# Performance work log

Hardware: AMD Instinct MI355X
Metric: run time of the kernel (lower is better)

The kernel has to match this reference:

```python
import jax, jax.numpy as jnp
import numpy as np

G, S, F, H, C, L = 32, 2048, 128, 128, 40, 3
N = G * S           # 65536 nodes
E = N * 16          # 1048576 edges


def setup_inputs() -> dict:
    key = jax.random.key(0)
    ks = jax.random.split(key, 10)
    x = jax.random.normal(ks[0], (N, F), dtype=jnp.float32)
    edge_index = jax.random.randint(ks[1], (2, E), 0, N, dtype=jnp.int64)
    E_meta = jax.random.normal(ks[2], (G, H), dtype=jnp.float32)
    ptr = (jnp.arange(G + 1, dtype=jnp.int64) * S)  # uniform partitions
    # learned params (xavier-ish scaling)
    w0 = jax.random.normal(ks[3], (F, 1), dtype=jnp.float32) * (2.0 / (F + 1)) ** 0.5
    b0 = jax.random.normal(ks[4], (F, H), dtype=jnp.float32) * (2.0 / (F + H)) ** 0.5
    conv_w = jax.random.normal(ks[5], (L, H, H), dtype=jnp.float32) * (1.0 / H) ** 0.5
    conv_b = jnp.zeros((L, H), dtype=jnp.float32)
    lt1_w = jax.random.normal(ks[6], (C, H), dtype=jnp.float32) * (1.0 / H) ** 0.5
    lt1_b = jnp.zeros((C,), dtype=jnp.float32)
    return {"x": x, "edge_index": edge_index, "E_meta": E_meta, "ptr": ptr,
            "w0": w0, "b0": b0, "conv_w": conv_w, "conv_b": conv_b,
            "lt1_w": lt1_w, "lt1_b": lt1_b}


def _gcn_conv(h, src, dst, deg_inv_sqrt, W, b):
    # GCNConv (PyG defaults): h' = D^-1/2 (A+I) D^-1/2 (h W) + b
    hw = h @ W                                          # [N,H]
    norm = deg_inv_sqrt[src] * deg_inv_sqrt[dst]        # [E+N]
    msg = hw[src] * norm[:, None]                       # gather + scale
    return jax.ops.segment_sum(msg, dst, num_segments=h.shape[0]) + b


def reference(x, edge_index, E_meta, ptr, w0, b0, conv_w, conv_b, lt1_w, lt1_b):
    n_nodes = x.shape[0]
    g = E_meta.shape[0]
    s = n_nodes // g  # uniform ptr (ptr[i] = i*s) by construction
    # per-partition dynamic weight: relu(w0 @ emb^T + b0) -> [G,F,H]
    Wdyn = jax.nn.relu(w0[None, :, :] * E_meta[:, None, :] + b0[None, :, :])
    # segment matmul x[ptr[i]:ptr[i+1]] @ Wdyn[i], concatenated -> [N,H]
    h = jnp.einsum('gsf,gfh->gsh', x.reshape(g, s, -1), Wdyn).reshape(n_nodes, -1)
    # add self loops once; symmetric normalization on target degree
    loop = jnp.arange(n_nodes, dtype=edge_index.dtype)
    src = jnp.concatenate([edge_index[0], loop])
    dst = jnp.concatenate([edge_index[1], loop])
    deg = jax.ops.segment_sum(jnp.ones_like(dst, dtype=h.dtype), dst,
                              num_segments=n_nodes)
    deg_inv_sqrt = jnp.where(deg > 0, jax.lax.rsqrt(deg), 0.0)
    for l in range(conv_w.shape[0]):
        h = jax.nn.relu(_gcn_conv(h, src, dst, deg_inv_sqrt, conv_w[l], conv_b[l]))
        # F.dropout with training=False is identity (eval mode)
    logits = h @ lt1_w.T + lt1_b
    return jax.nn.log_softmax(logits, axis=1)
```

## Files before the change

kernel.cpp:

```cpp
#include <hip/hip_runtime.h>

#define NNODES 65536
#define NEDGES 1048576
#define HDIM 128
#define NCLS 40
#define BCAP 6144

#define FP8_SCALE 32.0f
#define FP8_INV   0.03125f

typedef unsigned int uint;
typedef __attribute__((ext_vector_type(8))) short bf16x8;
typedef __attribute__((ext_vector_type(4))) float f32x4;
typedef __attribute__((ext_vector_type(2))) float f32x2;

__device__ __forceinline__ float bf_lo(uint v) {
    return __builtin_bit_cast(float, v << 16);
}
__device__ __forceinline__ float bf_hi(uint v) {
    return __builtin_bit_cast(float, v & 0xffff0000u);
}
__device__ __forceinline__ uint pack_bf16x2(float a, float b) {
    uint ua = __builtin_bit_cast(uint, a);
    uint ub = __builtin_bit_cast(uint, b);
    ua += 0x7fff + ((ua >> 16) & 1);
    ub += 0x7fff + ((ub >> 16) & 1);
    return (ua >> 16) | (ub & 0xffff0000u);
}
__device__ __forceinline__ float tobf(float v) {
    uint u = __builtin_bit_cast(uint, v);
    u += 0x7fff + ((u >> 16) & 1);
    return __builtin_bit_cast(float, u & 0xffff0000u);
}

__device__ __forceinline__ f32x2 fp8_pair(uint u) {
    return __builtin_amdgcn_cvt_pk_f32_fp8((int)u, false);
}

__global__ __launch_bounds__(256) void convT_kernel(
    const float* __restrict__ cw, uint* __restrict__ WT, int* __restrict__ gcursor,
    const float* __restrict__ ltw, uint* __restrict__ WcT8)
{
    int t = threadIdx.x;
    if (blockIdx.x == 0) gcursor[t] = 0;
    int idx = blockIdx.x * 256 + t;
    if (idx < 24576) {
        int ip = idx & 63;
        int o = (idx >> 6) & 127;
        int l = idx >> 13;
        int i0 = ip * 2;
        float v0 = cw[l * 16384 + i0 * 128 + o];
        float v1 = cw[l * 16384 + (i0 + 1) * 128 + o];
        WT[idx] = pack_bf16x2(v0, v1);
    } else {
        int idx2 = idx - 24576;
        int part = (idx2 >= 3072) ? 1 : 0;
        int r = idx2 - part * 3072;
        int o = r >> 6;
        int ip = r & 63;
        float v0 = 0.f, v1 = 0.f;
        if (o < NCLS) {
            float w0v = ltw[o * 128 + ip * 2];
            float w1v = ltw[o * 128 + ip * 2 + 1];
            float h0 = tobf(w0v), h1 = tobf(w1v);
            if (part == 0) { v0 = h0; v1 = h1; }
            else { v0 = w0v - h0; v1 = w1v - h1; }
        }
        WcT8[idx2] = pack_bf16x2(v0, v1);
    }
}

__global__ __launch_bounds__(256) void bucket_scatter(
    const int* __restrict__ src, const int* __restrict__ dst,
    int* __restrict__ gcursor, uint* __restrict__ binned)
{
    __shared__ int lcnt[256];
    __shared__ int lbase[256];
    int t = threadIdx.x;
    int base = blockIdx.x * 4096;
    lcnt[t] = 0;
    __syncthreads();
    uint e[16];
#pragma unroll
    for (int k = 0; k < 16; k++) {
        int i = base + k * 256 + t;
        uint s = (uint)src[i];
        uint d = (uint)dst[i];
        e[k] = (d << 16) | s;
        atomicAdd(&lcnt[d >> 8], 1);
    }
    __syncthreads();
    lbase[t] = t * BCAP + atomicAdd(&gcursor[t], lcnt[t]);
    lcnt[t] = 0;
    __syncthreads();
#pragma unroll
    for (int k = 0; k < 16; k++) {
        int b = e[k] >> 24;
        int r = atomicAdd(&lcnt[b], 1);
        binned[lbase[b] + r] = e[k];
    }
}

__global__ __launch_bounds__(256) void prep_kernel(
    const uint* __restrict__ binned, const int* __restrict__ gcursor,
    int* __restrict__ row_beg, int* __restrict__ row_end4,
    float* __restrict__ dis, int* __restrict__ csr,
    const float* __restrict__ w0, const float* __restrict__ em,
    const float* __restrict__ b0, const uint* __restrict__ convwT0,
    uint* __restrict__ WT)
{
    __shared__ int cnt[256];
    __shared__ int tmp[256];
    __shared__ int fb[256];
    const int t = threadIdx.x;

    if (blockIdx.x < 256) {
        int b = blockIdx.x;
        int e0 = b * BCAP, e1 = e0 + gcursor[b];
        cnt[t] = 0;
        __syncthreads();
        for (int i = e0 + t; i < e1; i += 256)
            atomicAdd(&cnt[(binned[i] >> 16) & 255], 1);
        __syncthreads();
        int v = cnt[t];
        int size4 = (v + 3) & ~3;
        tmp[t] = size4;
        __syncthreads();
        for (int off = 1; off < 256; off <<= 1) {
            int u = (t >= off) ? tmp[t - off] : 0;
            __syncthreads();
            tmp[t] += u;
            __syncthreads();
        }
        fb[t] = tmp[t] - size4;
        int node = (b << 8) + t;
        int beg = e0 + fb[t];
        row_beg[node] = beg;
        row_end4[node] = beg + size4;
        dis[node] = rsqrtf((float)(v + 1));
        for (int p = v; p < size4; p++) csr[beg + p] = NNODES;
        cnt[t] = 0;
        __syncthreads();
        for (int i = e0 + t; i < e1; i += 256) {
            uint e = binned[i];
            int d = (e >> 16) & 255;
            int r = atomicAdd(&cnt[d], 1);
            csr[e0 + fb[d] + r] = (int)(e & 0xffffu);
        }
    } else {
        int bb = blockIdx.x - 256;
        const int g = bb >> 3;
        const int c = bb & 7;
        const int wave = t >> 6;
        const int lane = t & 63;
        const int q = lane >> 4;
        const int l16 = lane & 15;
        const float* emg = em + g * 128;

        f32x4 acc[2];
#pragma unroll
        for (int r = 0; r < 2; r++) {
            acc[r][0] = 0.f; acc[r][1] = 0.f; acc[r][2] = 0.f; acc[r][3] = 0.f;
        }
        const int f = c * 16 + l16;
        const float wf = w0[f];

#pragma unroll
        for (int k0 = 0; k0 < 128; k0 += 32) {
            const int kf = k0 + q * 8;
            bf16x8 afrag[2];
#pragma unroll
            for (int r = 0; r < 2; r++) {
                uint4 u = *(const uint4*)(convwT0 +
                    (size_t)(wave * 32 + r * 16 + l16) * 64 + (kf >> 1));
                afrag[r] = __builtin_bit_cast(bf16x8, u);
            }
            float4 e0 = *(const float4*)(emg + kf);
            float4 e1 = *(const float4*)(emg + kf + 4);
            const float* bp = b0 + (size_t)f * 128 + kf;
            float4 bb0 = *(const float4*)bp;
            float4 bb1 = *(const float4*)(bp + 4);
            float v0 = fmaxf(fmaf(wf, e0.x, bb0.x), 0.f);
            float v1 = fmaxf(fmaf(wf, e0.y, bb0.y), 0.f);
            float v2 = fmaxf(fmaf(wf, e0.z, bb0.z), 0.f);
            float v3 = fmaxf(fmaf(wf, e0.w, bb0.w), 0.f);
            float v4 = fmaxf(fmaf(wf, e1.x, bb1.x), 0.f);
            float v5 = fmaxf(fmaf(wf, e1.y, bb1.y), 0.f);
            float v6 = fmaxf(fmaf(wf, e1.z, bb1.z), 0.f);
            float v7 = fmaxf(fmaf(wf, e1.w, bb1.w), 0.f);
            uint4 u;
            u.x = pack_bf16x2(v0, v1);
            u.y = pack_bf16x2(v2, v3);
            u.z = pack_bf16x2(v4, v5);
            u.w = pack_bf16x2(v6, v7);
            bf16x8 bfrag = __builtin_bit_cast(bf16x8, u);
#pragma unroll
            for (int r = 0; r < 2; r++)
                acc[r] = __builtin_amdgcn_mfma_f32_16x16x32_bf16(
                    afrag[r], bfrag, acc[r], 0, 0, 0);
        }

        uint* WTg = WT + (size_t)g * 8192;
#pragma unroll
        for (int r = 0; r < 2; r++) {
            int o0 = wave * 32 + r * 16 + q * 4;
#pragma unroll
            for (int i = 0; i < 4; i++) {
                int o = o0 + i;
                float v = acc[r][i];
                float w = __shfl_xor(v, 1);
                uint p = (lane & 1) ? pack_bf16x2(w, v) : pack_bf16x2(v, w);
                if (!(lane & 1))
                    WTg[(size_t)o * 64 + (uint)(f >> 1)] = p;
            }
        }
    }
}

__device__ __forceinline__ void store_fp8_row(
    uint* __restrict__ Cp8, int row, float s32, const f32x4* accRC,
    int lane, int l16, int i)
{
#pragma unroll
    for (int c = 0; c < 8; c++) {
        float v = accRC[c][i] * s32;
        float w = __shfl_xor(v, 1);
        int us = __builtin_amdgcn_cvt_pk_fp8_f32(v, w, 0, false);
        uint partner = (uint)__shfl_xor(us, 2);
        if ((lane & 3) == 0) {
            uint p = ((uint)us & 0xffffu) | (partner << 16);
            Cp8[(size_t)row * 32 + c * 4 + (l16 >> 2)] = p;
        }
    }
}

__global__ __launch_bounds__(256) void gemm_mfma(
    const float* __restrict__ A, const uint* __restrict__ BT,
    uint* __restrict__ Cp8, const float* __restrict__ dis, int perGroup)
{
    const int t = threadIdx.x;
    const int wave = t >> 6;
    const int lane = t & 63;
    const int q = lane >> 4;
    const int l16 = lane & 15;
    const int rowBase = blockIdx.x * 128;
    const uint* Bp = perGroup ? BT + ((size_t)(rowBase >> 11) << 13) : BT;

    if (blockIdx.x == 0 && t < 32)
        Cp8[(size_t)NNODES * 32 + t] = 0u;

    f32x4 acc[2][8];
#pragma unroll
    for (int r = 0; r < 2; r++)
#pragma unroll
        for (int c = 0; c < 8; c++) {
            acc[r][c][0] = 0.f; acc[r][c][1] = 0.f;
            acc[r][c][2] = 0.f; acc[r][c][3] = 0.f;
        }

    const int mBase = rowBase + wave * 32 + l16;

#pragma unroll
    for (int k0 = 0; k0 < 128; k0 += 32) {
        const int kf = k0 + q * 8;
        bf16x8 afrag[2];
#pragma unroll
        for (int r = 0; r < 2; r++) {
            const float* ap = A + (size_t)(mBase + r * 16) * 128 + kf;
            float4 a0 = *(const float4*)ap;
            float4 a1 = *(const float4*)(ap + 4);
            uint4 u;
            u.x = pack_bf16x2(a0.x, a0.y);
            u.y = pack_bf16x2(a0.z, a0.w);
            u.z = pack_bf16x2(a1.x, a1.y);
            u.w = pack_bf16x2(a1.z, a1.w);
            afrag[r] = __builtin_bit_cast(bf16x8, u);
        }
#pragma unroll
        for (int c = 0; c < 8; c++) {
            uint4 u = *(const uint4*)(Bp + (size_t)(c * 16 + l16) * 64 + (kf >> 1));
            bf16x8 bfrag = __builtin_bit_cast(bf16x8, u);
#pragma unroll
            for (int r = 0; r < 2; r++)
                acc[r][c] = __builtin_amdgcn_mfma_f32_16x16x32_bf16(
                    afrag[r], bfrag, acc[r][c], 0, 0, 0);
        }
    }

#pragma unroll
    for (int r = 0; r < 2; r++) {
        int row0 = rowBase + wave * 32 + r * 16 + q * 4;
#pragma unroll
        for (int i = 0; i < 4; i++) {
            int row = row0 + i;
            float s32 = dis[row] * FP8_SCALE;
            store_fp8_row(Cp8, row, s32, acc[r], lane, l16, i);
        }
    }
}

__device__ __forceinline__ void aggregate_quarter(
    const uint* __restrict__ hws8_in, const int* __restrict__ row_beg,
    const int* __restrict__ row_end4, const int* __restrict__ csr,
    const float* __restrict__ dis, const float* __restrict__ bias,
    uint* __restrict__ hT, int rowBase, int wave, int lane)
{
    const int q = lane >> 4;
    const int s = lane & 15;
    const float4 bv0 = *(const float4*)(bias + s * 8);
    const float4 bv1 = *(const float4*)(bias + s * 8 + 4);
#pragma unroll
    for (int j = 0; j < 4; j++) {
        const int nl = wave * 16 + j * 4 + q;
        const int n = rowBase + nl;
        const int beg = row_beg[n];
        const int end4 = row_end4[n];
        int mx = (end4 - beg) >> 2;
        mx = max(mx, __shfl_xor(mx, 16));
        mx = max(mx, __shfl_xor(mx, 32));
        uint2 su = *((const uint2*)(hws8_in + (size_t)n * 32) + s);
        f32x2 a0 = fp8_pair(su.x), a1 = fp8_pair(su.x >> 16);
        f32x2 a2 = fp8_pair(su.y), a3 = fp8_pair(su.y >> 16);
        f32x2 b0 = {0.f, 0.f}, b1 = {0.f, 0.f};
        f32x2 b2 = {0.f, 0.f}, b3 = {0.f, 0.f};
        int i = beg;
        for (int it = 0; it < mx; it += 2, i += 8) {
            int4 sA = *(const int4*)(csr + i);
            int4 sB = *(const int4*)(csr + i + 4);
            if (i >= end4) { sA.x = NNODES; sA.y = NNODES; sA.z = NNODES; sA.w = NNODES; }
            if (i + 4 >= end4) { sB.x = NNODES; sB.y = NNODES; sB.z = NNODES; sB.w = NNODES; }
            uint2 u0 = *((const uint2*)(hws8_in + (size_t)sA.x * 32) + s);
            uint2 u1 = *((const uint2*)(hws8_in + (size_t)sA.y * 32) + s);
            uint2 u2 = *((const uint2*)(hws8_in + (size_t)sA.z * 32) + s);
            uint2 u3 = *((const uint2*)(hws8_in + (size_t)sA.w * 32) + s);
            uint2 u4 = *((const uint2*)(hws8_in + (size_t)sB.x * 32) + s);
            uint2 u5 = *((const uint2*)(hws8_in + (size_t)sB.y * 32) + s);
            uint2 u6 = *((const uint2*)(hws8_in + (size_t)sB.z * 32) + s);
            uint2 u7 = *((const uint2*)(hws8_in + (size_t)sB.w * 32) + s);
            a0 += fp8_pair(u0.x); a1 += fp8_pair(u0.x >> 16);
            a2 += fp8_pair(u0.y); a3 += fp8_pair(u0.y >> 16);
            b0 += fp8_pair(u1.x); b1 += fp8_pair(u1.x >> 16);
            b2 += fp8_pair(u1.y); b3 += fp8_pair(u1.y >> 16);
            a0 += fp8_pair(u2.x); a1 += fp8_pair(u2.x >> 16);
            a2 += fp8_pair(u2.y); a3 += fp8_pair(u2.y >> 16);
            b0 += fp8_pair(u3.x); b1 += fp8_pair(u3.x >> 16);
            b2 += fp8_pair(u3.y); b3 += fp8_pair(u3.y >> 16);
            a0 += fp8_pair(u4.x); a1 += fp8_pair(u4.x >> 16);
            a2 += fp8_pair(u4.y); a3 += fp8_pair(u4.y >> 16);
            b0 += fp8_pair(u5.x); b1 += fp8_pair(u5.x >> 16);
            b2 += fp8_pair(u5.y); b3 += fp8_pair(u5.y >> 16);
            a0 += fp8_pair(u6.x); a1 += fp8_pair(u6.x >> 16);
            a2 += fp8_pair(u6.y); a3 += fp8_pair(u6.y >> 16);
            b0 += fp8_pair(u7.x); b1 += fp8_pair(u7.x >> 16);
            b2 += fp8_pair(u7.y); b3 += fp8_pair(u7.y >> 16);
        }
        a0 += b0; a1 += b1; a2 += b2; a3 += b3;
        const float d = dis[n] * FP8_INV;
        float o0 = fmaxf(fmaf(d, a0.x, bv0.x), 0.f);
        float o1 = fmaxf(fmaf(d, a0.y, bv0.y), 0.f);
        float o2 = fmaxf(fmaf(d, a1.x, bv0.z), 0.f);
        float o3 = fmaxf(fmaf(d, a1.y, bv0.w), 0.f);
        float o4 = fmaxf(fmaf(d, a2.x, bv1.x), 0.f);
        float o5 = fmaxf(fmaf(d, a2.y, bv1.y), 0.f);
        float o6 = fmaxf(fmaf(d, a3.x, bv1.z), 0.f);
        float o7 = fmaxf(fmaf(d, a3.y, bv1.w), 0.f);
        uint4 w;
        w.x = pack_bf16x2(o0, o1);
        w.y = pack_bf16x2(o2, o3);
        w.z = pack_bf16x2(o4, o5);
        w.w = pack_bf16x2(o6, o7);
        *(uint4*)&hT[nl * 68 + s * 4] = w;
    }
}

__global__ __launch_bounds__(512) void agg_gemm_kernel(
    const uint* __restrict__ hws8_in, const int* __restrict__ row_beg,
    const int* __restrict__ row_end4, const int* __restrict__ csr,
    const float* __restrict__ dis, const float* __restrict__ bias,
    const uint* __restrict__ BT, uint* __restrict__ out8)
{
    __shared__ uint hT[128 * 68];
    const int t = threadIdx.x;
    const int wave = t >> 6;
    const int lane = t & 63;
    const int rowBase = blockIdx.x * 128;

    if (blockIdx.x == 0 && t < 32)
        out8[(size_t)NNODES * 32 + t] = 0u;

    aggregate_quarter(hws8_in, row_beg, row_end4, csr, dis, bias,
                      hT, rowBase, wave, lane);
    __syncthreads();

    const int q = lane >> 4;
    const int l16 = lane & 15;
    const int mw = wave & 3;
    const int nw = wave >> 2;

    f32x4 acc[2][4];
#pragma unroll
    for (int r = 0; r < 2; r++)
#pragma unroll
        for (int c = 0; c < 4; c++) {
            acc[r][c][0] = 0.f; acc[r][c][1] = 0.f;
            acc[r][c][2] = 0.f; acc[r][c][3] = 0.f;
        }

#pragma unroll
    for (int k0 = 0; k0 < 128; k0 += 32) {
        const int kp = (k0 >> 1) + q * 4;
        bf16x8 afrag[2];
#pragma unroll
        for (int r = 0; r < 2; r++) {
            uint4 u = *(const uint4*)&hT[(mw * 32 + r * 16 + l16) * 68 + kp];
            afrag[r] = __builtin_bit_cast(bf16x8, u);
        }
#pragma unroll
        for (int c = 0; c < 4; c++) {
            uint4 u = *(const uint4*)(BT +
                (size_t)(nw * 64 + c * 16 + l16) * 64 + kp);
            bf16x8 bfrag = __builtin_bit_cast(bf16x8, u);
#pragma unroll
            for (int r = 0; r < 2; r++)
                acc[r][c] = __builtin_amdgcn_mfma_f32_16x16x32_bf16(
                    afrag[r], bfrag, acc[r][c], 0, 0, 0);
        }
    }

#pragma unroll
    for (int r = 0; r < 2; r++) {
        int row0 = rowBase + mw * 32 + r * 16 + q * 4;
#pragma unroll
        for (int i = 0; i < 4; i++) {
            int row = row0 + i;
            float s32 = dis[row] * FP8_SCALE;
#pragma unroll
            for (int c = 0; c < 4; c++) {
                float v = acc[r][c][i] * s32;
                float w = __shfl_xor(v, 1);
                int us = __builtin_amdgcn_cvt_pk_fp8_f32(v, w, 0, false);
                uint partner = (uint)__shfl_xor(us, 2);
                if ((lane & 3) == 0) {
                    uint p = ((uint)us & 0xffffu) | (partner << 16);
                    out8[(size_t)row * 32 + (nw * 4 + c) * 4 + (l16 >> 2)] = p;
                }
            }
        }
    }
}

__global__ __launch_bounds__(512) void agg_logits_kernel(
    const uint* __restrict__ hws8_in, const int* __restrict__ row_beg,
    const int* __restrict__ row_end4, const int* __restrict__ csr,
    const float* __restrict__ dis, const float* __restrict__ bias,
    const uint* __restrict__ WcT8, const float* __restrict__ bc,
    float* __restrict__ out)
{
    __shared__ uint hT[128 * 68];
    const int t = threadIdx.x;
    const int wave = t >> 6;
    const int lane = t & 63;
    const int rowBase = blockIdx.x * 128;

    aggregate_quarter(hws8_in, row_beg, row_end4, csr, dis, bias,
                      hT, rowBase, wave, lane);
    __syncthreads();

    const int q = lane >> 4;
    const int l16 = lane & 15;

    f32x4 acc[3];
#pragma unroll
    for (int c = 0; c < 3; c++) {
        acc[c][0] = 0.f; acc[c][1] = 0.f; acc[c][2] = 0.f; acc[c][3] = 0.f;
    }

#pragma unroll
    for (int k0 = 0; k0 < 128; k0 += 32) {
        const int kp = (k0 >> 1) + q * 4;
        uint4 ua = *(const uint4*)&hT[(wave * 16 + l16) * 68 + kp];
        bf16x8 af = __builtin_bit_cast(bf16x8, ua);
#pragma unroll
        for (int tile = 0; tile < 3; tile++) {
            uint4 uh = *(const uint4*)(WcT8 + (size_t)(tile * 16 + l16) * 64 + kp);
            uint4 ul = *(const uint4*)(WcT8 + (size_t)(48 + tile * 16 + l16) * 64 + kp);
            acc[tile] = __builtin_amdgcn_mfma_f32_16x16x32_bf16(
                af, __builtin_bit_cast(bf16x8, uh), acc[tile], 0, 0, 0);
            acc[tile] = __builtin_amdgcn_mfma_f32_16x16x32_bf16(
                af, __builtin_bit_cast(bf16x8, ul), acc[tile], 0, 0, 0);
        }
    }

    const float bt0 = bc[l16];
    const float bt1 = bc[16 + l16];
    const float bt2 = (l16 < 8) ? bc[32 + l16] : 0.f;

#pragma unroll
    for (int i = 0; i < 4; i++) {
        const int node = rowBase + wave * 16 + q * 4 + i;
        float g0 = acc[0][i] + bt0;
        float g1 = acc[1][i] + bt1;
        float g2 = (l16 < 8) ? (acc[2][i] + bt2) : -1e30f;
        float m = fmaxf(fmaxf(g0, g1), g2);
        for (int off = 1; off < 16; off <<= 1) m = fmaxf(m, __shfl_xor(m, off));
        float sum = expf(g0 - m) + expf(g1 - m) + ((l16 < 8) ? expf(g2 - m) : 0.f);
        for (int off = 1; off < 16; off <<= 1) sum += __shfl_xor(sum, off);
        float lse = m + logf(sum);
        float* on = out + (size_t)node * NCLS;
        on[l16] = g0 - lse;
        on[16 + l16] = g1 - lse;
        if (l16 < 8) on[32 + l16] = g2 - lse;
    }
}

extern "C" void kernel_launch(void* const* d_in, const int* in_sizes, int n_in,
                              void* d_out, int out_size, void* d_ws, size_t ws_size,
                              hipStream_t stream)
{
    const float* x     = (const float*)d_in[0];
    const int*   ei    = (const int*)d_in[1];
    const float* em    = (const float*)d_in[2];
    const float* w0    = (const float*)d_in[4];
    const float* b0    = (const float*)d_in[5];
    const float* convw = (const float*)d_in[6];
    const float* convb = (const float*)d_in[7];
    const float* ltw   = (const float*)d_in[8];
    const float* ltb   = (const float*)d_in[9];
    float* out = (float*)d_out;

    char* ws = (char*)d_ws;
    size_t off = 0;
    auto alloc = [&](size_t bytes) -> void* {
        void* p = ws + off;
        off += (bytes + 255) & ~(size_t)255;
        return p;
    };
    uint*  hws8A    = (uint*)alloc((size_t)(NNODES + 1) * 32 * 4);
    uint*  hws8B    = (uint*)alloc((size_t)(NNODES + 1) * 32 * 4);
    uint*  WcombT   = (uint*)alloc((size_t)32 * 128 * 64 * 4);
    uint*  convwT   = (uint*)alloc((size_t)3 * 128 * 64 * 4);
    uint*  WcT8     = (uint*)alloc((size_t)96 * 64 * 4);
    int*   gcursor  = (int*)alloc(256 * 4);
    uint*  binned   = (uint*)alloc((size_t)256 * BCAP * 4);
    int*   row_beg  = (int*)alloc((size_t)NNODES * 4);
    int*   row_end4 = (int*)alloc((size_t)NNODES * 4);
    float* dis      = (float*)alloc((size_t)NNODES * 4);
    int*   csr      = (int*)alloc((size_t)256 * BCAP * 4);

    const int* esrc = ei;
    const int* edst = ei + NEDGES;

    convT_kernel<<<120, 256, 0, stream>>>(convw, convwT, gcursor, ltw, WcT8);
    bucket_scatter<<<NEDGES / 4096, 256, 0, stream>>>(esrc, edst, gcursor, binned);
    prep_kernel<<<512, 256, 0, stream>>>(binned, gcursor, row_beg, row_end4, dis,
                                         csr, w0, em, b0, convwT, WcombT);

    gemm_mfma<<<NNODES / 128, 256, 0, stream>>>(x, WcombT, hws8A, dis, 1);

    agg_gemm_kernel<<<NNODES / 128, 512, 0, stream>>>(
        hws8A, row_beg, row_end4, csr, dis, convb + 0 * 128,
        convwT + (size_t)1 * 8192, hws8B);
    agg_gemm_kernel<<<NNODES / 128, 512, 0, stream>>>(
        hws8B, row_beg, row_end4, csr, dis, convb + 1 * 128,
        convwT + (size_t)2 * 8192, hws8A);
    agg_logits_kernel<<<NNODES / 128, 512, 0, stream>>>(
        hws8A, row_beg, row_end4, csr, dis, convb + 2 * 128, WcT8, ltb, out);
}
```

Measured before the change: 236.1 us.

## Aggregate one node per eight lanes with 16-byte gathers, halve rows per block

The aggregation step now has each group of 8 lanes own one node and load 16 bytes per neighbor row. Before, 16 lanes each loaded 8 bytes per node and each wave looped over 4 nodes. Blocks now cover 64 rows instead of 128, so the grid doubles and the per-wave MFMA tile shrinks. The goal is wider gather loads and more blocks to hide memory latency, at the cost of doubling the reads of the B weights per node. In the logits kernel, half the waves now sit idle during the GEMM phase.

```diff
diff --git a/kernel.cpp b/kernel.cpp
--- a/kernel.cpp
+++ b/kernel.cpp
@@ -299,78 +299,88 @@
     }
 }
 
-__device__ __forceinline__ void aggregate_quarter(
+__device__ __forceinline__ void aggregate_eighth(
     const uint* __restrict__ hws8_in, const int* __restrict__ row_beg,
     const int* __restrict__ row_end4, const int* __restrict__ csr,
     const float* __restrict__ dis, const float* __restrict__ bias,
     uint* __restrict__ hT, int rowBase, int wave, int lane)
 {
-    const int q = lane >> 4;
-    const int s = lane & 15;
-    const float4 bv0 = *(const float4*)(bias + s * 8);
-    const float4 bv1 = *(const float4*)(bias + s * 8 + 4);
-#pragma unroll
-    for (int j = 0; j < 4; j++) {
-        const int nl = wave * 16 + j * 4 + q;
-        const int n = rowBase + nl;
-        const int beg = row_beg[n];
-        const int end4 = row_end4[n];
-        int mx = (end4 - beg) >> 2;
-        mx = max(mx, __shfl_xor(mx, 16));
-        mx = max(mx, __shfl_xor(mx, 32));
-        uint2 su = *((const uint2*)(hws8_in + (size_t)n * 32) + s);
-        f32x2 a0 = fp8_pair(su.x), a1 = fp8_pair(su.x >> 16);
-        f32x2 a2 = fp8_pair(su.y), a3 = fp8_pair(su.y >> 16);
-        f32x2 b0 = {0.f, 0.f}, b1 = {0.f, 0.f};
-        f32x2 b2 = {0.f, 0.f}, b3 = {0.f, 0.f};
-        int i = beg;
-        for (int it = 0; it < mx; it += 2, i += 8) {
-            int4 sA = *(const int4*)(csr + i);
-            int4 sB = *(const int4*)(csr + i + 4);
-            if (i >= end4) { sA.x = NNODES; sA.y = NNODES; sA.z = NNODES; sA.w = NNODES; }
-            if (i + 4 >= end4) { sB.x = NNODES; sB.y = NNODES; sB.z = NNODES; sB.w = NNODES; }
-            uint2 u0 = *((const uint2*)(hws8_in + (size_t)sA.x * 32) + s);
-            uint2 u1 = *((const uint2*)(hws8_in + (size_t)sA.y * 32) + s);
-            uint2 u2 = *((const uint2*)(hws8_in + (size_t)sA.z * 32) + s);
-            uint2 u3 = *((const uint2*)(hws8_in + (size_t)sA.w * 32) + s);
-            uint2 u4 = *((const uint2*)(hws8_in + (size_t)sB.x * 32) + s);
-            uint2 u5 = *((const uint2*)(hws8_in + (size_t)sB.y * 32) + s);
-            uint2 u6 = *((const uint2*)(hws8_in + (size_t)sB.z * 32) + s);
-            uint2 u7 = *((const uint2*)(hws8_in + (size_t)sB.w * 32) + s);
-            a0 += fp8_pair(u0.x); a1 += fp8_pair(u0.x >> 16);
-            a2 += fp8_pair(u0.y); a3 += fp8_pair(u0.y >> 16);
-            b0 += fp8_pair(u1.x); b1 += fp8_pair(u1.x >> 16);
-            b2 += fp8_pair(u1.y); b3 += fp8_pair(u1.y >> 16);
-            a0 += fp8_pair(u2.x); a1 += fp8_pair(u2.x >> 16);
-            a2 += fp8_pair(u2.y); a3 += fp8_pair(u2.y >> 16);
-            b0 += fp8_pair(u3.x); b1 += fp8_pair(u3.x >> 16);
-            b2 += fp8_pair(u3.y); b3 += fp8_pair(u3.y >> 16);
-            a0 += fp8_pair(u4.x); a1 += fp8_pair(u4.x >> 16);
-            a2 += fp8_pair(u4.y); a3 += fp8_pair(u4.y >> 16);
-            b0 += fp8_pair(u5.x); b1 += fp8_pair(u5.x >> 16);
-            b2 += fp8_pair(u5.y); b3 += fp8_pair(u5.y >> 16);
-            a0 += fp8_pair(u6.x); a1 += fp8_pair(u6.x >> 16);
-            a2 += fp8_pair(u6.y); a3 += fp8_pair(u6.y >> 16);
-            b0 += fp8_pair(u7.x); b1 += fp8_pair(u7.x >> 16);
-            b2 += fp8_pair(u7.y); b3 += fp8_pair(u7.y >> 16);
-        }
-        a0 += b0; a1 += b1; a2 += b2; a3 += b3;
-        const float d = dis[n] * FP8_INV;
-        float o0 = fmaxf(fmaf(d, a0.x, bv0.x), 0.f);
-        float o1 = fmaxf(fmaf(d, a0.y, bv0.y), 0.f);
-        float o2 = fmaxf(fmaf(d, a1.x, bv0.z), 0.f);
-        float o3 = fmaxf(fmaf(d, a1.y, bv0.w), 0.f);
-        float o4 = fmaxf(fmaf(d, a2.x, bv1.x), 0.f);
-        float o5 = fmaxf(fmaf(d, a2.y, bv1.y), 0.f);
-        float o6 = fmaxf(fmaf(d, a3.x, bv1.z), 0.f);
-        float o7 = fmaxf(fmaf(d, a3.y, bv1.w), 0.f);
-        uint4 w;
-        w.x = pack_bf16x2(o0, o1);
-        w.y = pack_bf16x2(o2, o3);
-        w.z = pack_bf16x2(o4, o5);
-        w.w = pack_bf16x2(o6, o7);
-        *(uint4*)&hT[nl * 68 + s * 4] = w;
-    }
+    const int g = lane >> 3;
+    const int s = lane & 7;
+    const int nl = wave * 8 + g;
+    const int n = rowBase + nl;
+    const int beg = row_beg[n];
+    const int end4 = row_end4[n];
+    int mx = (end4 - beg) >> 2;
+    mx = max(mx, __shfl_xor(mx, 8));
+    mx = max(mx, __shfl_xor(mx, 16));
+    mx = max(mx, __shfl_xor(mx, 32));
+
+    uint4 su = *((const uint4*)(hws8_in + (size_t)n * 32) + s);
+    f32x2 a[8];
+    a[0] = fp8_pair(su.x); a[1] = fp8_pair(su.x >> 16);
+    a[2] = fp8_pair(su.y); a[3] = fp8_pair(su.y >> 16);
+    a[4] = fp8_pair(su.z); a[5] = fp8_pair(su.z >> 16);
+    a[6] = fp8_pair(su.w); a[7] = fp8_pair(su.w >> 16);
+
+#define ACC8(u) do { \
+        a[0] += fp8_pair((u).x); a[1] += fp8_pair((u).x >> 16); \
+        a[2] += fp8_pair((u).y); a[3] += fp8_pair((u).y >> 16); \
+        a[4] += fp8_pair((u).z); a[5] += fp8_pair((u).z >> 16); \
+        a[6] += fp8_pair((u).w); a[7] += fp8_pair((u).w >> 16); } while (0)
+
+    int i = beg;
+    for (int it = 0; it < mx; it += 2, i += 8) {
+        int4 sA = *(const int4*)(csr + i);
+        int4 sB = *(const int4*)(csr + i + 4);
+        if (i >= end4) { sA.x = NNODES; sA.y = NNODES; sA.z = NNODES; sA.w = NNODES; }
+        if (i + 4 >= end4) { sB.x = NNODES; sB.y = NNODES; sB.z = NNODES; sB.w = NNODES; }
+        uint4 u0 = *((const uint4*)(hws8_in + (size_t)sA.x * 32) + s);
+        uint4 u1 = *((const uint4*)(hws8_in + (size_t)sA.y * 32) + s);
+        uint4 u2 = *((const uint4*)(hws8_in + (size_t)sA.z * 32) + s);
+        uint4 u3 = *((const uint4*)(hws8_in + (size_t)sA.w * 32) + s);
+        uint4 u4 = *((const uint4*)(hws8_in + (size_t)sB.x * 32) + s);
+        uint4 u5 = *((const uint4*)(hws8_in + (size_t)sB.y * 32) + s);
+        uint4 u6 = *((const uint4*)(hws8_in + (size_t)sB.z * 32) + s);
+        uint4 u7 = *((const uint4*)(hws8_in + (size_t)sB.w * 32) + s);
+        ACC8(u0); ACC8(u1); ACC8(u2); ACC8(u3);
+        ACC8(u4); ACC8(u5); ACC8(u6); ACC8(u7);
+    }
+#undef ACC8
+
+    const float d = dis[n] * FP8_INV;
+    const float* bp = bias + s * 16;
+    float4 b0 = *(const float4*)bp;
+    float4 b1 = *(const float4*)(bp + 4);
+    float4 b2 = *(const float4*)(bp + 8);
+    float4 b3 = *(const float4*)(bp + 12);
+    float o0  = fmaxf(fmaf(d, a[0].x, b0.x), 0.f);
+    float o1  = fmaxf(fmaf(d, a[0].y, b0.y), 0.f);
+    float o2  = fmaxf(fmaf(d, a[1].x, b0.z), 0.f);
+    float o3  = fmaxf(fmaf(d, a[1].y, b0.w), 0.f);
+    float o4  = fmaxf(fmaf(d, a[2].x, b1.x), 0.f);
+    float o5  = fmaxf(fmaf(d, a[2].y, b1.y), 0.f);
+    float o6  = fmaxf(fmaf(d, a[3].x, b1.z), 0.f);
+    float o7  = fmaxf(fmaf(d, a[3].y, b1.w), 0.f);
+    float o8  = fmaxf(fmaf(d, a[4].x, b2.x), 0.f);
+    float o9  = fmaxf(fmaf(d, a[4].y, b2.y), 0.f);
+    float o10 = fmaxf(fmaf(d, a[5].x, b2.z), 0.f);
+    float o11 = fmaxf(fmaf(d, a[5].y, b2.w), 0.f);
+    float o12 = fmaxf(fmaf(d, a[6].x, b3.x), 0.f);
+    float o13 = fmaxf(fmaf(d, a[6].y, b3.y), 0.f);
+    float o14 = fmaxf(fmaf(d, a[7].x, b3.z), 0.f);
+    float o15 = fmaxf(fmaf(d, a[7].y, b3.w), 0.f);
+    uint4 w0, w1;
+    w0.x = pack_bf16x2(o0, o1);
+    w0.y = pack_bf16x2(o2, o3);
+    w0.z = pack_bf16x2(o4, o5);
+    w0.w = pack_bf16x2(o6, o7);
+    w1.x = pack_bf16x2(o8, o9);
+    w1.y = pack_bf16x2(o10, o11);
+    w1.z = pack_bf16x2(o12, o13);
+    w1.w = pack_bf16x2(o14, o15);
+    *(uint4*)&hT[nl * 68 + s * 8] = w0;
+    *(uint4*)&hT[nl * 68 + s * 8 + 4] = w1;
 }
 
 __global__ __launch_bounds__(512) void agg_gemm_kernel(
@@ -379,29 +389,29 @@
     const float* __restrict__ dis, const float* __restrict__ bias,
     const uint* __restrict__ BT, uint* __restrict__ out8)
 {
-    __shared__ uint hT[128 * 68];
+    __shared__ uint hT[64 * 68];
     const int t = threadIdx.x;
     const int wave = t >> 6;
     const int lane = t & 63;
-    const int rowBase = blockIdx.x * 128;
+    const int rowBase = blockIdx.x * 64;
 
     if (blockIdx.x == 0 && t < 32)
         out8[(size_t)NNODES * 32 + t] = 0u;
 
-    aggregate_quarter(hws8_in, row_beg, row_end4, csr, dis, bias,
-                      hT, rowBase, wave, lane);
+    aggregate_eighth(hws8_in, row_beg, row_end4, csr, dis, bias,
+                     hT, rowBase, wave, lane);
     __syncthreads();
 
     const int q = lane >> 4;
     const int l16 = lane & 15;
-    const int mw = wave & 3;
-    const int nw = wave >> 2;
-
-    f32x4 acc[2][4];
+    const int mw = wave & 1;
+    const int nw = wave >> 1;
+
+    f32x4 acc[2][2];
 #pragma unroll
     for (int r = 0; r < 2; r++)
 #pragma unroll
-        for (int c = 0; c < 4; c++) {
+        for (int c = 0; c < 2; c++) {
             acc[r][c][0] = 0.f; acc[r][c][1] = 0.f;
             acc[r][c][2] = 0.f; acc[r][c][3] = 0.f;
         }
@@ -416,9 +426,9 @@
             afrag[r] = __builtin_bit_cast(bf16x8, u);
         }
 #pragma unroll
-        for (int c = 0; c < 4; c++) {
+        for (int c = 0; c < 2; c++) {
             uint4 u = *(const uint4*)(BT +
-                (size_t)(nw * 64 + c * 16 + l16) * 64 + kp);
+                (size_t)(nw * 32 + c * 16 + l16) * 64 + kp);
             bf16x8 bfrag = __builtin_bit_cast(bf16x8, u);
 #pragma unroll
             for (int r = 0; r < 2; r++)
@@ -435,14 +445,14 @@
             int row = row0 + i;
             float s32 = dis[row] * FP8_SCALE;
 #pragma unroll
-            for (int c = 0; c < 4; c++) {
+            for (int c = 0; c < 2; c++) {
                 float v = acc[r][c][i] * s32;
                 float w = __shfl_xor(v, 1);
                 int us = __builtin_amdgcn_cvt_pk_fp8_f32(v, w, 0, false);
                 uint partner = (uint)__shfl_xor(us, 2);
                 if ((lane & 3) == 0) {
                     uint p = ((uint)us & 0xffffu) | (partner << 16);
-                    out8[(size_t)row * 32 + (nw * 4 + c) * 4 + (l16 >> 2)] = p;
+                    out8[(size_t)row * 32 + (nw * 2 + c) * 4 + (l16 >> 2)] = p;
                 }
             }
         }
@@ -456,15 +466,17 @@
     const uint* __restrict__ WcT8, const float* __restrict__ bc,
     float* __restrict__ out)
 {
-    __shared__ uint hT[128 * 68];
+    __shared__ uint hT[64 * 68];
     const int t = threadIdx.x;
     const int wave = t >> 6;
     const int lane = t & 63;
-    const int rowBase = blockIdx.x * 128;
-
-    aggregate_quarter(hws8_in, row_beg, row_end4, csr, dis, bias,
-                      hT, rowBase, wave, lane);
+    const int rowBase = blockIdx.x * 64;
+
+    aggregate_eighth(hws8_in, row_beg, row_end4, csr, dis, bias,
+                     hT, rowBase, wave, lane);
     __syncthreads();
+
+    if (wave >= 4) return;
 
     const int q = lane >> 4;
     const int l16 = lane & 15;
@@ -557,12 +569,12 @@
 
     gemm_mfma<<<NNODES / 128, 256, 0, stream>>>(x, WcombT, hws8A, dis, 1);
 
-    agg_gemm_kernel<<<NNODES / 128, 512, 0, stream>>>(
+    agg_gemm_kernel<<<NNODES / 64, 512, 0, stream>>>(
         hws8A, row_beg, row_end4, csr, dis, convb + 0 * 128,
         convwT + (size_t)1 * 8192, hws8B);
-    agg_gemm_kernel<<<NNODES / 128, 512, 0, stream>>>(
+    agg_gemm_kernel<<<NNODES / 64, 512, 0, stream>>>(
         hws8B, row_beg, row_end4, csr, dis, convb + 1 * 128,
         convwT + (size_t)2 * 8192, hws8A);
-    agg_logits_kernel<<<NNODES / 128, 512, 0, stream>>>(
+    agg_logits_kernel<<<NNODES / 64, 512, 0, stream>>>(
         hws8A, row_beg, row_end4, csr, dis, convb + 2 * 128, WcT8, ltb, out);
 }
```

After: 240.6 us. Within noise of the previous version (+1.9%).
